# Performance work log

Hardware: AMD Instinct MI355X
Metric: run time of the kernel (lower is better)

## Reference

```python
import jax, jax.numpy as jnp
import numpy as np

B, E, V, T, NSTEP = 32, 256, 32000, 2048, 128  # batch, embed_dim, graph_dim, total_length, min_len


def setup_inputs() -> dict:
    key = jax.random.key(0)
    k1, k2, k3, k4 = jax.random.split(key, 4)
    latent = jax.random.normal(k1, (T, E * E), dtype=jnp.float32) * 0.02
    vocab_w = jax.random.normal(k2, (E, V), dtype=jnp.float32) * 0.02
    vocab_b = jnp.zeros((V,), dtype=jnp.float32)
    zi = jax.random.randint(k3, (B,), 0, T)
    y = jax.random.randint(k4, (B, NSTEP), 0, V)
    return {"latent": latent, "vocab_w": vocab_w, "vocab_b": vocab_b, "zi": zi, "y": y}


def _trajectory(z_flat, n_step):
    # z_flat: [B, E*E] -> per-sample transition matrix [B, E, E]
    trans = z_flat.reshape(-1, E, E)
    z0 = trans[:, 0, :]  # seed state = first row, [B, E]

    def step(z, _):
        # torch .std() is unbiased (ddof=1)
        zn = z / (1e-5 + jnp.std(z, axis=-1, keepdims=True, ddof=1)) * 0.113
        emit = jnp.einsum('be,bef->bf', zn, trans)  # [B, E]
        return emit, emit

    _, zs = jax.lax.scan(step, z0, None, length=n_step)  # [n_step, B, E]
    return jnp.transpose(zs, (1, 0, 2))  # [B, n_step, E]


def reference(latent, vocab_w, vocab_b, zi, y):
    z = latent[zi]                      # [B, E*E]
    zs = _trajectory(z, NSTEP)          # [B, n_step, E]
    logits = zs @ vocab_w + vocab_b     # [B, n_step, V]
    logp = jax.nn.log_softmax(logits, axis=-1)
    yp = jnp.take_along_axis(logp, y[..., None], axis=-1)[..., 0]  # [B, n_step]
    return yp
```

## Files before the change

kernel.cpp:

```cpp
#include <hip/hip_runtime.h>
#include <hip/hip_bf16.h>

#define BATCH 32
#define E 256
#define V 32000
#define NSTEP 128
#define M_TOTAL (BATCH * NSTEP)
#define BM 128
#define BN2 128
#define NBT (V / BN2)
#define NGRP 16
#define NPART (2 * NGRP)

typedef __attribute__((ext_vector_type(4))) float f32x4;
typedef __attribute__((ext_vector_type(2))) float f32x2;
typedef __attribute__((ext_vector_type(8))) short s16x8;
typedef __attribute__((ext_vector_type(4))) unsigned int u32x4;

static __device__ __forceinline__ short f2bf(float v) {
    __hip_bfloat16 h = __float2bfloat16(v);
    return *reinterpret_cast<short*>(&h);
}

static __device__ __forceinline__ unsigned char f2fp8(float v) {
    int p = __builtin_amdgcn_cvt_pk_fp8_f32(v, v, 0, false);
    return (unsigned char)(p & 0xff);
}
template<bool HI>
static __device__ __forceinline__ f32x2 fp8x2_to_f32(unsigned int x) {
    return __builtin_amdgcn_cvt_pk_f32_fp8((int)x, HI);
}

static __device__ __forceinline__ int fragpos(int e) {
    return ((e >> 3) & 3) * 64 + (e >> 5) * 8 + (e & 7);
}

static __device__ __forceinline__ long long ll2(unsigned int a, unsigned int b) {
    return (long long)(((unsigned long long)b << 32) | a);
}

static __device__ __forceinline__ void gload_lds16(const void* g, void* l) {
    __builtin_amdgcn_global_load_lds((const __attribute__((address_space(1))) void*)g,
                                     (__attribute__((address_space(3))) void*)l,
                                     16, 0, 0);
}

template<int CTRL>
static __device__ __forceinline__ float dpp_add(float v) {
    int i = __builtin_amdgcn_update_dpp(0, __builtin_bit_cast(int, v), CTRL, 0xF, 0xF, false);
    return v + __builtin_bit_cast(float, i);
}
static __device__ __forceinline__ float row16_sum(float v) {
    v = dpp_add<0x121>(v);
    v = dpp_add<0x122>(v);
    v = dpp_add<0x124>(v);
    v = dpp_add<0x128>(v);
    return v;
}

__global__ __launch_bounds__(512, 2) void traj_transpose_kernel(
        const float* __restrict__ latent, const int* __restrict__ zi,
        const float* __restrict__ w,
        unsigned char* __restrict__ zsb8, unsigned char* __restrict__ wt8) {
    __shared__ float tile[64][65];
    __shared__ __align__(16) short zsh[2][E];
    __shared__ __align__(16) float red[2][16];

    const int tid = threadIdx.x;

    if (blockIdx.x >= BATCH) {
        const int bb = blockIdx.x - BATCH;
        const int k0 = (bb & 3) * 64;
        const int n0 = (bb >> 2) * 64;
        const int c  = tid & 63;
        const int r8 = tid >> 6;
        #pragma unroll
        for (int r = r8; r < 64; r += 8)
            tile[r][c] = w[(size_t)(k0 + r) * V + n0 + c];
        __syncthreads();
        const int fp = fragpos(k0 + c);
        #pragma unroll
        for (int r = r8; r < 64; r += 8)
            wt8[(size_t)(n0 + r) * E + fp] = f2fp8(tile[c][r]);
        return;
    }

    const int b    = blockIdx.x;
    const int lane = tid & 63;
    const int wv   = tid >> 6;
    const int lm   = lane & 15;
    const int g    = lane >> 4;
    const float* tr = latent + (size_t)zi[b] * (E * E);

    s16x8 bfrag[2][8];
    #pragma unroll
    for (int nt = 0; nt < 2; ++nt)
        #pragma unroll
        for (int kk = 0; kk < 8; ++kk) {
            s16x8 fr;
            #pragma unroll
            for (int j = 0; j < 8; ++j)
                fr[j] = f2bf(tr[(size_t)(kk * 32 + g * 8 + j) * E + wv * 32 + nt * 16 + lm]);
            bfrag[nt][kk] = fr;
        }

    if (tid < E) zsh[0][tid] = f2bf(tr[tid]);

    {
        float v = (tid < E) ? tr[tid] : 0.f;
        float a = row16_sum(v), a2 = row16_sum(v * v);
        a  += __shfl_xor(a, 16);  a2 += __shfl_xor(a2, 16);
        a  += __shfl_xor(a, 32);  a2 += __shfl_xor(a2, 32);
        if (lane == 0) { red[1][wv] = a; red[1][8 + wv] = a2; }
    }
    __syncthreads();

    float scale;
    {
        f32x4 p0 = *(const f32x4*)&red[1][0], p1 = *(const f32x4*)&red[1][4];
        f32x4 q0 = *(const f32x4*)&red[1][8], q1 = *(const f32x4*)&red[1][12];
        float ts  = (p0[0]+p0[1]+p0[2]+p0[3]) + (p1[0]+p1[1]+p1[2]+p1[3]);
        float ts2 = (q0[0]+q0[1]+q0[2]+q0[3]) + (q1[0]+q1[1]+q1[2]+q1[3]);
        float var = fmaxf((ts2 - ts * ts * (1.0f / 256.0f)) * (1.0f / 255.0f), 0.f);
        scale = 0.113f / (1e-5f + sqrtf(var));
    }

    const int p0i = fragpos(wv * 32 + lm);
    const int p1i = fragpos(wv * 32 + 16 + lm);

    for (int t = 0; t < NSTEP; ++t) {
        const short* zrd = zsh[t & 1];
        s16x8 a[8];
        #pragma unroll
        for (int kk = 0; kk < 8; ++kk)
            a[kk] = *(const s16x8*)((const char*)zrd + kk * 64 + g * 16);

        f32x4 acc0 = {}, acc1 = {};
        #pragma unroll
        for (int kk = 0; kk < 8; ++kk) {
            acc0 = __builtin_amdgcn_mfma_f32_16x16x32_bf16(a[kk], bfrag[0][kk], acc0, 0, 0, 0);
            acc1 = __builtin_amdgcn_mfma_f32_16x16x32_bf16(a[kk], bfrag[1][kk], acc1, 0, 0, 0);
        }

        const float e0 = scale * acc0[0], e1 = scale * acc1[0];
        if (g == 0) {
            zsh[(t + 1) & 1][wv * 32 + lm]      = f2bf(e0);
            zsh[(t + 1) & 1][wv * 32 + 16 + lm] = f2bf(e1);
            unsigned char* zr = zsb8 + ((size_t)b * NSTEP + t) * E;
            zr[p0i] = f2fp8(e0);
            zr[p1i] = f2fp8(e1);
        }

        float u  = row16_sum(acc0[0] + acc1[0]);
        float u2 = row16_sum(acc0[0] * acc0[0] + acc1[0] * acc1[0]);
        if (lane == 0) { red[t & 1][wv] = u; red[t & 1][8 + wv] = u2; }
        __syncthreads();

        const float* rd = red[t & 1];
        f32x4 r0 = *(const f32x4*)&rd[0], r1 = *(const f32x4*)&rd[4];
        f32x4 s0 = *(const f32x4*)&rd[8], s1 = *(const f32x4*)&rd[12];
        float ts  = (r0[0]+r0[1]+r0[2]+r0[3]) + (r1[0]+r1[1]+r1[2]+r1[3]);
        float ts2 = (s0[0]+s0[1]+s0[2]+s0[3]) + (s1[0]+s1[1]+s1[2]+s1[3]);
        float var = fmaxf((ts2 - ts * ts * (1.0f / 256.0f)) * (1.0f / 255.0f), 0.f);
        scale = 0.113f / (1e-5f + scale * sqrtf(var));
    }
}

__global__ __launch_bounds__(256, 2) void gemm_lse_kernel(const unsigned char* __restrict__ zsb8,
                                                          const unsigned char* __restrict__ wt8,
                                                          const float* __restrict__ vb,
                                                          float* __restrict__ partial) {
    __shared__ unsigned char bpan[2][BN2 * E];

    const int tid  = threadIdx.x;
    const int lane = tid & 63;
    const int w    = tid >> 6;
    const int bm   = blockIdx.x >> 4;
    const int grp  = blockIdx.x & 15;
    const int m0   = bm * BM;
    const int t0   = (NBT * grp) >> 4;
    const int t1   = (NBT * (grp + 1)) >> 4;

    const int wr = w >> 1, wc = w & 1;
    const int lm = lane & 15, lk = lane >> 4;
    const int mw = m0 + wr * 64;

    long long areg[4][8];
    #pragma unroll
    for (int rt = 0; rt < 4; ++rt)
        #pragma unroll
        for (int kp = 0; kp < 4; ++kp) {
            u32x4 v = *(const u32x4*)(zsb8 + (size_t)(mw + rt * 16 + lm) * E + lk * 64 + kp * 16);
            areg[rt][2 * kp]     = ll2(v[0], v[1]);
            areg[rt][2 * kp + 1] = ll2(v[2], v[3]);
        }

    {
        const size_t gbase = (size_t)(t0 * BN2) * E;
        #pragma unroll
        for (int i = 0; i < 8; ++i) {
            const int c   = i * 256 + tid;
            const int row = c >> 4;
            const int gsl = ((c & 15) - row) & 15;
            gload_lds16(wt8 + gbase + (size_t)row * E + gsl * 16, (char*)bpan[0] + c * 16);
        }
    }

    float rs[4][4] = {};

    __syncthreads();

    for (int i = t0; i < t1; ++i) {
        const int cur = (i - t0) & 1;
        if (i + 1 < t1) {
            const size_t gbase = (size_t)((i + 1) * BN2) * E;
            #pragma unroll
            for (int j = 0; j < 8; ++j) {
                const int c   = j * 256 + tid;
                const int row = c >> 4;
                const int gsl = ((c & 15) - row) & 15;
                gload_lds16(wt8 + gbase + (size_t)row * E + gsl * 16,
                            (char*)bpan[cur ^ 1] + c * 16);
            }
        }

        const int n0 = i * BN2;
        float bias[4];
        #pragma unroll
        for (int nt = 0; nt < 4; ++nt) bias[nt] = vb[n0 + wc * 64 + nt * 16 + lm];

        f32x4 acc[4][4] = {};
        const unsigned char* bp = bpan[cur];
        #pragma unroll
        for (int kp = 0; kp < 4; ++kp) {
            long long blo[4], bhi[4];
            #pragma unroll
            for (int nt = 0; nt < 4; ++nt) {
                const int rn   = wc * 64 + nt * 16 + lm;
                const int slot = (lk * 4 + kp + rn) & 15;
                u32x4 bv = *(const u32x4*)(bp + rn * 256 + slot * 16);
                blo[nt] = ll2(bv[0], bv[1]);
                bhi[nt] = ll2(bv[2], bv[3]);
            }
            #pragma unroll
            for (int rt = 0; rt < 4; ++rt)
                #pragma unroll
                for (int nt = 0; nt < 4; ++nt)
                    acc[rt][nt] = __builtin_amdgcn_mfma_f32_16x16x32_fp8_fp8(
                        areg[rt][2 * kp], blo[nt], acc[rt][nt], 0, 0, 0);
            #pragma unroll
            for (int rt = 0; rt < 4; ++rt)
                #pragma unroll
                for (int nt = 0; nt < 4; ++nt)
                    acc[rt][nt] = __builtin_amdgcn_mfma_f32_16x16x32_fp8_fp8(
                        areg[rt][2 * kp + 1], bhi[nt], acc[rt][nt], 0, 0, 0);
        }

        #pragma unroll
        for (int rt = 0; rt < 4; ++rt)
            #pragma unroll
            for (int nt = 0; nt < 4; ++nt)
                #pragma unroll
                for (int r = 0; r < 4; ++r)
                    rs[rt][r] += __expf(acc[rt][nt][r] + bias[nt]);

        __syncthreads();
    }

    const int cr = lane >> 4;
    #pragma unroll
    for (int rt = 0; rt < 4; ++rt)
        #pragma unroll
        for (int r = 0; r < 4; ++r) {
            const float v = row16_sum(rs[rt][r]);
            if (lm == 0)
                partial[(size_t)(grp * 2 + wc) * M_TOTAL + mw + rt * 16 + cr * 4 + r] = v;
        }
}

__global__ __launch_bounds__(256) void finalize_kernel(const unsigned char* __restrict__ zsb8,
                                                       const unsigned char* __restrict__ wt8,
                                                       const float* __restrict__ vb,
                                                       const int* __restrict__ y,
                                                       const float* __restrict__ partial,
                                                       float* __restrict__ out) {
    const int tid  = threadIdx.x;
    const int lane = tid & 63;
    const int rw   = lane >> 4;
    const int kl   = lane & 15;
    const int row  = blockIdx.x * 16 + (tid >> 6) * 4 + rw;
    const int yrow = y[row];

    u32x4 za = *(const u32x4*)(zsb8 + (size_t)row * E + kl * 16);
    u32x4 wa = *(const u32x4*)(wt8 + (size_t)yrow * E + kl * 16);
    float acc = 0.f;
    #pragma unroll
    for (int q = 0; q < 4; ++q) {
        f32x2 a0 = fp8x2_to_f32<false>(za[q]), b0 = fp8x2_to_f32<false>(wa[q]);
        f32x2 a1 = fp8x2_to_f32<true>(za[q]),  b1 = fp8x2_to_f32<true>(wa[q]);
        acc += a0[0] * b0[0] + a0[1] * b0[1] + a1[0] * b1[0] + a1[1] * b1[1];
    }
    const float logit = row16_sum(acc) + vb[yrow];

    float ps = partial[(size_t)kl * M_TOTAL + row] + partial[(size_t)(kl + 16) * M_TOTAL + row];
    const float tot = row16_sum(ps);

    if (kl == 0) out[row] = logit - logf(tot);
}

extern "C" void kernel_launch(void* const* d_in, const int* in_sizes, int n_in,
                              void* d_out, int out_size, void* d_ws, size_t ws_size,
                              hipStream_t stream) {
    const float* latent  = (const float*)d_in[0];
    const float* vocab_w = (const float*)d_in[1];
    const float* vocab_b = (const float*)d_in[2];
    const int*   zi      = (const int*)d_in[3];
    const int*   y       = (const int*)d_in[4];
    float* out = (float*)d_out;

    char* ws = (char*)d_ws;
    float*         partial = (float*)(ws);
    unsigned char* zsb8    = (unsigned char*)(ws + 524288);
    unsigned char* wt8     = (unsigned char*)(ws + 524288 + 1048576);

    hipLaunchKernelGGL(traj_transpose_kernel, dim3(BATCH + 4 * (V / 64)), dim3(512), 0, stream,
                       latent, zi, vocab_w, zsb8, wt8);
    hipLaunchKernelGGL(gemm_lse_kernel, dim3(32 * NGRP), dim3(256), 0, stream,
                       zsb8, wt8, vocab_b, partial);
    hipLaunchKernelGGL(finalize_kernel, dim3(M_TOTAL / 16), dim3(256), 0, stream,
                       zsb8, wt8, vocab_b, y, partial, out);
}
```

Measured before the change: 152.8 us.

## Pipeline exp epilogue with next tile MFMA using 512-thread blocks

Restructures the fused GEMM plus log-sum-exp kernel into 512-thread blocks of 8 waves. Each wave now covers 64x32 of the tile, and each block covers twice as many vocab tiles, so there are half as many blocks. The exp accumulation for one tile is delayed and interleaved with the MFMAs of the next tile, using two alternating accumulator sets, so transcendental and matrix work can overlap. It also replaces __expf with exp2 on pre-scaled inputs. In exchange, B-fragment reuse per wave drops and register pressure from the double accumulators goes up.

```diff
diff --git a/kernel.cpp b/kernel.cpp
--- a/kernel.cpp
+++ b/kernel.cpp
@@ -9,8 +9,8 @@
 #define BM 128
 #define BN2 128
 #define NBT (V / BN2)
-#define NGRP 16
-#define NPART (2 * NGRP)
+#define NGRP 8
+#define L2E 1.4426950408889634f
 
 typedef __attribute__((ext_vector_type(4))) float f32x4;
 typedef __attribute__((ext_vector_type(2))) float f32x2;
@@ -166,22 +166,23 @@
     }
 }
 
-__global__ __launch_bounds__(256, 2) void gemm_lse_kernel(const unsigned char* __restrict__ zsb8,
+__global__ __launch_bounds__(512, 2) void gemm_lse_kernel(const unsigned char* __restrict__ zsb8,
                                                           const unsigned char* __restrict__ wt8,
                                                           const float* __restrict__ vb,
                                                           float* __restrict__ partial) {
-    __shared__ unsigned char bpan[2][BN2 * E];
+    __shared__ unsigned char bpan0[BN2 * E];
+    __shared__ unsigned char bpan1[BN2 * E];
 
     const int tid  = threadIdx.x;
     const int lane = tid & 63;
     const int w    = tid >> 6;
-    const int bm   = blockIdx.x >> 4;
-    const int grp  = blockIdx.x & 15;
+    const int grp  = blockIdx.x & 7;
+    const int bm   = blockIdx.x >> 3;
     const int m0   = bm * BM;
-    const int t0   = (NBT * grp) >> 4;
-    const int t1   = (NBT * (grp + 1)) >> 4;
-
-    const int wr = w >> 1, wc = w & 1;
+    const int t0   = (NBT * grp) >> 3;
+    const int t1   = (NBT * (grp + 1)) >> 3;
+
+    const int wr = w >> 2, wc = w & 3;
     const int lm = lane & 15, lk = lane >> 4;
     const int mw = m0 + wr * 64;
 
@@ -195,77 +196,91 @@
             areg[rt][2 * kp + 1] = ll2(v[2], v[3]);
         }
 
-    {
-        const size_t gbase = (size_t)(t0 * BN2) * E;
-        #pragma unroll
-        for (int i = 0; i < 8; ++i) {
-            const int c   = i * 256 + tid;
+    float rs[4][4] = {};
+
+    auto STAGE = [&](int tile, unsigned char* dst) {
+        const size_t gbase = (size_t)(tile * BN2) * E;
+        #pragma unroll
+        for (int j = 0; j < 4; ++j) {
+            const int c   = j * 512 + tid;
             const int row = c >> 4;
             const int gsl = ((c & 15) - row) & 15;
-            gload_lds16(wt8 + gbase + (size_t)row * E + gsl * 16, (char*)bpan[0] + c * 16);
-        }
-    }
-
-    float rs[4][4] = {};
-
-    __syncthreads();
-
-    for (int i = t0; i < t1; ++i) {
-        const int cur = (i - t0) & 1;
-        if (i + 1 < t1) {
-            const size_t gbase = (size_t)((i + 1) * BN2) * E;
-            #pragma unroll
-            for (int j = 0; j < 8; ++j) {
-                const int c   = j * 256 + tid;
-                const int row = c >> 4;
-                const int gsl = ((c & 15) - row) & 15;
-                gload_lds16(wt8 + gbase + (size_t)row * E + gsl * 16,
-                            (char*)bpan[cur ^ 1] + c * 16);
-            }
-        }
-
-        const int n0 = i * BN2;
-        float bias[4];
-        #pragma unroll
-        for (int nt = 0; nt < 4; ++nt) bias[nt] = vb[n0 + wc * 64 + nt * 16 + lm];
-
-        f32x4 acc[4][4] = {};
-        const unsigned char* bp = bpan[cur];
+            gload_lds16(wt8 + gbase + (size_t)row * E + gsl * 16, dst + c * 16);
+        }
+    };
+
+    auto COMPUTE = [&](const unsigned char* bp, f32x4 (&acc)[4][2], float (&bias)[2], int tile) {
+        const int n0 = tile * BN2;
+        bias[0] = vb[n0 + wc * 32 + lm] * L2E;
+        bias[1] = vb[n0 + wc * 32 + 16 + lm] * L2E;
+        #pragma unroll
+        for (int rt = 0; rt < 4; ++rt) { acc[rt][0] = (f32x4){}; acc[rt][1] = (f32x4){}; }
         #pragma unroll
         for (int kp = 0; kp < 4; ++kp) {
-            long long blo[4], bhi[4];
-            #pragma unroll
-            for (int nt = 0; nt < 4; ++nt) {
-                const int rn   = wc * 64 + nt * 16 + lm;
+            long long blo[2], bhi[2];
+            #pragma unroll
+            for (int nt = 0; nt < 2; ++nt) {
+                const int rn   = wc * 32 + nt * 16 + lm;
                 const int slot = (lk * 4 + kp + rn) & 15;
                 u32x4 bv = *(const u32x4*)(bp + rn * 256 + slot * 16);
                 blo[nt] = ll2(bv[0], bv[1]);
                 bhi[nt] = ll2(bv[2], bv[3]);
             }
             #pragma unroll
-            for (int rt = 0; rt < 4; ++rt)
-                #pragma unroll
-                for (int nt = 0; nt < 4; ++nt)
-                    acc[rt][nt] = __builtin_amdgcn_mfma_f32_16x16x32_fp8_fp8(
-                        areg[rt][2 * kp], blo[nt], acc[rt][nt], 0, 0, 0);
-            #pragma unroll
-            for (int rt = 0; rt < 4; ++rt)
-                #pragma unroll
-                for (int nt = 0; nt < 4; ++nt)
-                    acc[rt][nt] = __builtin_amdgcn_mfma_f32_16x16x32_fp8_fp8(
-                        areg[rt][2 * kp + 1], bhi[nt], acc[rt][nt], 0, 0, 0);
-        }
-
+            for (int rt = 0; rt < 4; ++rt) {
+                acc[rt][0] = __builtin_amdgcn_mfma_f32_16x16x32_fp8_fp8(areg[rt][2 * kp], blo[0], acc[rt][0], 0, 0, 0);
+                acc[rt][1] = __builtin_amdgcn_mfma_f32_16x16x32_fp8_fp8(areg[rt][2 * kp], blo[1], acc[rt][1], 0, 0, 0);
+            }
+            #pragma unroll
+            for (int rt = 0; rt < 4; ++rt) {
+                acc[rt][0] = __builtin_amdgcn_mfma_f32_16x16x32_fp8_fp8(areg[rt][2 * kp + 1], bhi[0], acc[rt][0], 0, 0, 0);
+                acc[rt][1] = __builtin_amdgcn_mfma_f32_16x16x32_fp8_fp8(areg[rt][2 * kp + 1], bhi[1], acc[rt][1], 0, 0, 0);
+            }
+        }
+    };
+
+    auto EPI = [&](const f32x4 (&acc)[4][2], const float (&bias)[2]) {
         #pragma unroll
         for (int rt = 0; rt < 4; ++rt)
             #pragma unroll
-            for (int nt = 0; nt < 4; ++nt)
-                #pragma unroll
-                for (int r = 0; r < 4; ++r)
-                    rs[rt][r] += __expf(acc[rt][nt][r] + bias[nt]);
-
-        __syncthreads();
-    }
+            for (int r = 0; r < 4; ++r)
+                rs[rt][r] += __builtin_amdgcn_exp2f(acc[rt][0][r] * L2E + bias[0])
+                           + __builtin_amdgcn_exp2f(acc[rt][1][r] * L2E + bias[1]);
+    };
+
+    f32x4 accA[4][2], accB[4][2];
+    float biasA[2], biasB[2];
+
+    STAGE(t0, bpan0);
+    __syncthreads();
+    if (t0 + 1 < t1) STAGE(t0 + 1, bpan1);
+    COMPUTE(bpan0, accA, biasA, t0);
+    __syncthreads();
+
+    int i = t0 + 1;
+    bool lastA = true;
+    while (i < t1) {
+        {
+            const unsigned char* bp = ((i - t0) & 1) ? bpan1 : bpan0;
+            unsigned char*       st = ((i - t0) & 1) ? bpan0 : bpan1;
+            if (i + 1 < t1) STAGE(i + 1, st);
+            COMPUTE(bp, accB, biasB, i);
+            EPI(accA, biasA);
+            __syncthreads();
+            lastA = false; ++i;
+            if (i >= t1) break;
+        }
+        {
+            const unsigned char* bp = ((i - t0) & 1) ? bpan1 : bpan0;
+            unsigned char*       st = ((i - t0) & 1) ? bpan0 : bpan1;
+            if (i + 1 < t1) STAGE(i + 1, st);
+            COMPUTE(bp, accA, biasA, i);
+            EPI(accB, biasB);
+            __syncthreads();
+            lastA = true; ++i;
+        }
+    }
+    if (lastA) EPI(accA, biasA); else EPI(accB, biasB);
 
     const int cr = lane >> 4;
     #pragma unroll
@@ -274,7 +289,7 @@
         for (int r = 0; r < 4; ++r) {
             const float v = row16_sum(rs[rt][r]);
             if (lm == 0)
-                partial[(size_t)(grp * 2 + wc) * M_TOTAL + mw + rt * 16 + cr * 4 + r] = v;
+                partial[(size_t)(grp * 4 + wc) * M_TOTAL + mw + rt * 16 + cr * 4 + r] = v;
         }
 }
 
@@ -325,7 +340,7 @@
 
     hipLaunchKernelGGL(traj_transpose_kernel, dim3(BATCH + 4 * (V / 64)), dim3(512), 0, stream,
                        latent, zi, vocab_w, zsb8, wt8);
-    hipLaunchKernelGGL(gemm_lse_kernel, dim3(32 * NGRP), dim3(256), 0, stream,
+    hipLaunchKernelGGL(gemm_lse_kernel, dim3(32 * NGRP), dim3(512), 0, stream,
                        zsb8, wt8, vocab_b, partial);
     hipLaunchKernelGGL(finalize_kernel, dim3(M_TOTAL / 16), dim3(256), 0, stream,
                        zsb8, wt8, vocab_b, y, partial, out);
```

Measured after the change: 151.9 us. Within noise of the previous version (-0.6%).
